# Kernel tuning notes

Measured on AMD Instinct MI355X. Metric: run time of the kernel, lower is better.

Reference implementation:

```python
import jax, jax.numpy as jnp
import numpy as np

B, I, O, G, D = 2048, 128, 128, 8, 2  # batch, input_dim, output_dim, num_grids, num_dim (complex algebra)
RHO = 1.0
EPS = 1e-5  # BatchNorm1d default eps
GRID_MIN, GRID_MAX = -2.0, 2.0


def _make_cayley():
    # Complex-number geometric algebra: metric=[-1], basis {1, e1}, e1*e1 = -1.
    # (a*b)_z = sum_{x,y} a_x b_y C[x,y,z]
    C = np.zeros((2, 2, 2), dtype=np.float32)
    C[0, 0, 0] = 1.0
    C[0, 1, 1] = 1.0
    C[1, 0, 1] = 1.0
    C[1, 1, 0] = -1.0
    return jnp.asarray(C)


def _make_grid():
    # create_grid2d_full: real varies along axis 0, imag along axis 1 -> (G, G, 2)
    g = jnp.linspace(GRID_MIN, GRID_MAX, G)
    gr, gi = jnp.meshgrid(g, g, indexing='ij')
    return jnp.stack((gr, gi), axis=-1)


def setup_inputs() -> dict:
    key = jax.random.key(0)
    k1, k2 = jax.random.split(key)
    x = jax.random.normal(k1, (B, I, D), dtype=jnp.float32)
    weights = jax.random.normal(k2, (I, O, G, G, D), dtype=jnp.float32)
    silu_weight = jnp.ones((I, O, D), dtype=jnp.float32)
    silu_bias = jnp.zeros((I, O, D), dtype=jnp.float32)
    gamma = jnp.ones((D,), dtype=jnp.float32)   # BatchNorm weight (componentwise)
    beta = jnp.zeros((D,), dtype=jnp.float32)   # BatchNorm bias
    return {
        'x': x,
        'weights': weights,
        'silu_weight': silu_weight,
        'silu_bias': silu_bias,
        'gamma': gamma,
        'beta': beta,
        'grid': _make_grid(),
        'cayley': _make_cayley(),
    }


def reference(x, weights, silu_weight, silu_bias, gamma, beta, grid, cayley):
    # RBF expansion: exp(-||x - grid_point||^2 / rho), complex-algebra norm^2 = a^2 + b^2
    diff = x[:, :, None, None, :] - grid[None, None, :, :, :]        # (B, I, G, G, D)
    rbf = jnp.exp(-jnp.sum(diff * diff, axis=-1) / RHO)              # (B, I, G, G)
    # grid-weight contraction
    res = jnp.einsum('biuv,iouvx->biox', rbf, weights)               # (B, I, O, D)
    # componentwise SiLU branch with Cayley-table (complex) multiplication
    s = jax.nn.silu(x)                                               # (B, I, D)
    sv = jnp.einsum('iox,biy,xyz->bioz', silu_weight, s, cayley)     # (B, I, O, D)
    sv = sv + silu_bias
    out = jnp.sum(res + sv, axis=1)                                  # (B, O, D) -- 'biox->box'
    # componentwise BatchNorm (training mode): stats over (B, O) per component
    mean = jnp.mean(out, axis=(0, 1))
    var = jnp.var(out, axis=(0, 1))
    out = gamma * (out - mean) * jax.lax.rsqrt(var + EPS) + beta
    return out
```

## Files before the change

### kernel.cpp

```cpp
#include <hip/hip_runtime.h>
#include <stdint.h>

typedef unsigned short u16;
typedef __attribute__((ext_vector_type(8))) short bf16x8;
typedef __attribute__((ext_vector_type(4))) float f32x4;

#define B_      2048
#define I_      128
#define O_      128
#define K_MAIN  8192
#define K_TOT   8448
#define N_      256
#define BO      262144

#define A_OFF      0u
#define A_BYTES    (2048u*8448u*2u)
#define W_OFF      (A_OFF + A_BYTES)
#define W_BYTES    (256u*8448u*2u)
#define OUTP_OFF   (W_OFF + W_BYTES)
#define OUTP_BYTES (524288u*4u)
#define BSUM_OFF   (OUTP_OFF + OUTP_BYTES)
#define STATS_OFF  (BSUM_OFF + 1024u)

__device__ __forceinline__ float bf2f(u16 u) {
    union { unsigned int i; float f; } c; c.i = ((unsigned int)u) << 16; return c.f;
}
__device__ __forceinline__ u16 f2bf(float f) {
    unsigned int u = __float_as_uint(f);
    return (u16)((u + 0x7fffu + ((u >> 16) & 1u)) >> 16);
}
__device__ __forceinline__ float loadF(const void* p, long idx, bool isbf) {
    return isbf ? bf2f(((const u16*)p)[idx]) : ((const float*)p)[idx];
}

#define GLD16(gsrc, ldst) __builtin_amdgcn_global_load_lds( \
    (const __attribute__((address_space(1))) void*)(gsrc),  \
    (__attribute__((address_space(3))) void*)(ldst), 16, 0, 0)

__global__ void zero_ws(float* out_pre, float* stats, float* bsum) {
    int gid = blockIdx.x * 256 + threadIdx.x;
    out_pre[gid] = 0.0f;
    if (gid < 256) bsum[gid] = 0.0f;
    if (gid < 4) stats[gid] = 0.0f;
}

__global__ __launch_bounds__(256) void pack_a(const void* x, const void* grd, u16* A,
                                              const u16* flag) {
    bool isbf = (flag[0] == 0x3F80u);
    __shared__ float sg[8];
    if (threadIdx.x < 8)
        sg[threadIdx.x] = loadF(grd, (long)threadIdx.x * 16, isbf);
    __syncthreads();
    int p = blockIdx.x * 256 + threadIdx.x;
    int b = p >> 7, i = p & 127;
    float xr = loadF(x, (long)p * 2, isbf);
    float xi = loadF(x, (long)p * 2 + 1, isbf);
    float er[8], ei[8];
#pragma unroll
    for (int j = 0; j < 8; ++j) {
        float dr = xr - sg[j]; er[j] = __expf(-dr * dr);
        float di = xi - sg[j]; ei[j] = __expf(-di * di);
    }
    unsigned int outp[32];
#pragma unroll
    for (int u = 0; u < 8; ++u)
#pragma unroll
        for (int v = 0; v < 8; v += 2) {
            unsigned int lo = f2bf(er[u] * ei[v]);
            unsigned int hi = f2bf(er[u] * ei[v + 1]);
            outp[(u * 8 + v) >> 1] = lo | (hi << 16);
        }
    u16* dst = A + (size_t)b * K_TOT + i * 64;
#pragma unroll
    for (int q = 0; q < 8; ++q)
        ((uint4*)dst)[q] = ((const uint4*)outp)[q];
    float s0 = xr / (1.0f + __expf(-xr));
    float s1 = xi / (1.0f + __expf(-xi));
    unsigned int packed = (unsigned int)f2bf(s0) | ((unsigned int)f2bf(s1) << 16);
    *(unsigned int*)(A + (size_t)b * K_TOT + K_MAIN + 2 * i) = packed;
}

__global__ __launch_bounds__(256) void pack_w(const void* wgt, const void* sw, u16* W,
                                              const u16* flag) {
    bool isbf = (flag[0] == 0x3F80u);
    if (blockIdx.x < 1024) {
        int gid = blockIdx.x * 256 + threadIdx.x;
        int t8 = gid & 15;
        int io = gid >> 4;
        int i = io >> 7, o = io & 127;
        int base = t8 * 8;
        int u = base >> 4, v0 = (base & 15) >> 1;
        long off = ((long)i * 128 + o) * 128 + base;
        float f[8];
        if (isbf) {
            uint4 raw = *(const uint4*)((const u16*)wgt + off);
            const u16* h = (const u16*)&raw;
#pragma unroll
            for (int j = 0; j < 8; ++j) f[j] = bf2f(h[j]);
        } else {
            float4 a = *(const float4*)((const float*)wgt + off);
            float4 bq = *(const float4*)((const float*)wgt + off + 4);
            f[0]=a.x; f[1]=a.y; f[2]=a.z; f[3]=a.w;
            f[4]=bq.x; f[5]=bq.y; f[6]=bq.z; f[7]=bq.w;
        }
        u16 re[4], im[4];
#pragma unroll
        for (int j = 0; j < 4; ++j) { re[j] = f2bf(f[2*j]); im[j] = f2bf(f[2*j+1]); }
        int k = i * 64 + u * 8 + v0;
        *(uint2*)&W[(size_t)(2*o)     * K_TOT + k] = *(const uint2*)re;
        *(uint2*)&W[(size_t)(2*o + 1) * K_TOT + k] = *(const uint2*)im;
    } else {
        int e = (blockIdx.x - 1024) * 256 + threadIdx.x;
        int n = e >> 8, j = e & 255;
        int o = n >> 1, xc = n & 1;
        int i = j >> 1, c = j & 1;
        float swr = loadF(sw, (long)(i * 128 + o) * 2, isbf);
        float swi = loadF(sw, (long)(i * 128 + o) * 2 + 1, isbf);
        float v = (xc == 0) ? (c == 0 ? swr : -swi) : (c == 0 ? swi : swr);
        W[(size_t)n * K_TOT + K_MAIN + j] = f2bf(v);
    }
}

__global__ void bias_sum(const void* sb, float* bsum, const u16* flag) {
    bool isbf = (flag[0] == 0x3F80u);
    int n = threadIdx.x;
    int i0 = blockIdx.x * 8;
    float s = 0.0f;
#pragma unroll
    for (int j = 0; j < 8; ++j) s += loadF(sb, (long)(i0 + j) * 256 + n, isbf);
    atomicAdd(&bsum[n], s);
}

#define BM 128
#define BN 64
#define BK 64
#define NSPLIT 8
#define KSTEPS 132

__global__ __launch_bounds__(256, 2) void gemm_k(const u16* __restrict__ A,
                                                 const u16* __restrict__ W,
                                                 float* out_pre) {
    __shared__ u16 As[BM * BK];
    __shared__ u16 Bs[BN * BK];
    int tid = threadIdx.x, lane = tid & 63, w = tid >> 6;
    int wm = w >> 1, wn = w & 1;
    int m0 = blockIdx.y * BM;
    int n0 = blockIdx.x * BN;
    int s = blockIdx.z;
    int kbeg = (KSTEPS * s) / NSPLIT, kend = (KSTEPS * (s + 1)) / NSPLIT;

    f32x4 zero = {0.f, 0.f, 0.f, 0.f};
    f32x4 acc[4][2];
#pragma unroll
    for (int mt = 0; mt < 4; ++mt)
#pragma unroll
        for (int nt = 0; nt < 2; ++nt) acc[mt][nt] = zero;

    int quad = lane >> 4, l16 = lane & 15;

    for (int kt = kbeg; kt < kend; ++kt) {
        int k0 = kt * BK;
#pragma unroll
        for (int j = 0; j < 4; ++j) {
            int c = (w * 4 + j) * 64 + lane;
            int row = c >> 3, col = c & 7;
            GLD16(A + (size_t)(m0 + row) * K_TOT + k0 + col * 8,
                  As + (size_t)(w * 4 + j) * 512);
        }
#pragma unroll
        for (int j = 0; j < 2; ++j) {
            int c = (w * 2 + j) * 64 + lane;
            int row = c >> 3, col = c & 7;
            GLD16(W + (size_t)(n0 + row) * K_TOT + k0 + col * 8,
                  Bs + (size_t)(w * 2 + j) * 512);
        }
        __syncthreads();
#pragma unroll
        for (int ks = 0; ks < 2; ++ks) {
            bf16x8 fa[4], fb[2];
#pragma unroll
            for (int mt = 0; mt < 4; ++mt)
                fa[mt] = *(const bf16x8*)&As[(wm * 64 + mt * 16 + l16) * BK + ks * 32 + quad * 8];
#pragma unroll
            for (int nt = 0; nt < 2; ++nt)
                fb[nt] = *(const bf16x8*)&Bs[(wn * 32 + nt * 16 + l16) * BK + ks * 32 + quad * 8];
#pragma unroll
            for (int mt = 0; mt < 4; ++mt)
#pragma unroll
                for (int nt = 0; nt < 2; ++nt)
                    acc[mt][nt] = __builtin_amdgcn_mfma_f32_16x16x32_bf16(
                        fa[mt], fb[nt], acc[mt][nt], 0, 0, 0);
        }
        __syncthreads();
    }
    int mbase = m0 + wm * 64 + quad * 4;
    int nbase = n0 + wn * 32 + l16;
#pragma unroll
    for (int mt = 0; mt < 4; ++mt)
#pragma unroll
        for (int nt = 0; nt < 2; ++nt) {
            int n = nbase + nt * 16;
#pragma unroll
            for (int r = 0; r < 4; ++r) {
                int m = mbase + mt * 16 + r;
                atomicAdd(&out_pre[(size_t)m * N_ + n], acc[mt][nt][r]);
            }
        }
}

__global__ void stats_k(const float* __restrict__ out_pre, const float* __restrict__ bsum,
                        float* stats) {
    int gid = blockIdx.x * 256 + threadIdx.x;
    int o = gid & 127;
    float vr = out_pre[(size_t)gid * 2]     + bsum[o * 2];
    float vi = out_pre[(size_t)gid * 2 + 1] + bsum[o * 2 + 1];
    float sr = vr, si = vi, qr = vr * vr, qi = vi * vi;
    for (int off = 32; off > 0; off >>= 1) {
        sr += __shfl_down(sr, off);
        si += __shfl_down(si, off);
        qr += __shfl_down(qr, off);
        qi += __shfl_down(qi, off);
    }
    __shared__ float red[4][4];
    int lane = threadIdx.x & 63, w = threadIdx.x >> 6;
    if (lane == 0) { red[w][0] = sr; red[w][1] = si; red[w][2] = qr; red[w][3] = qi; }
    __syncthreads();
    if (threadIdx.x < 4) {
        float t = red[0][threadIdx.x] + red[1][threadIdx.x] +
                  red[2][threadIdx.x] + red[3][threadIdx.x];
        atomicAdd(&stats[threadIdx.x], t);
    }
}

__global__ void norm_k(const float* __restrict__ out_pre, const float* __restrict__ bsum,
                       const float* __restrict__ stats, const void* gamma, const void* beta,
                       void* out, const u16* flag) {
    bool isbf = (flag[0] == 0x3F80u);
    int gid = blockIdx.x * 256 + threadIdx.x;
    int o = gid & 127;
    const float inv = 1.0f / (float)BO;
    float mr = stats[0] * inv, mi = stats[1] * inv;
    float varr = stats[2] * inv - mr * mr;
    float vari = stats[3] * inv - mi * mi;
    float gr = loadF(gamma, 0, isbf), gi = loadF(gamma, 1, isbf);
    float br = loadF(beta, 0, isbf),  bi = loadF(beta, 1, isbf);
    float scr = gr * rsqrtf(varr + 1e-5f);
    float sci = gi * rsqrtf(vari + 1e-5f);
    float vr = out_pre[(size_t)gid * 2]     + bsum[o * 2];
    float vi = out_pre[(size_t)gid * 2 + 1] + bsum[o * 2 + 1];
    float rr = (vr - mr) * scr + br;
    float ri = (vi - mi) * sci + bi;
    if (isbf) {
        unsigned int packed = (unsigned int)f2bf(rr) | ((unsigned int)f2bf(ri) << 16);
        *(unsigned int*)((u16*)out + (size_t)gid * 2) = packed;
    } else {
        ((float*)out)[(size_t)gid * 2]     = rr;
        ((float*)out)[(size_t)gid * 2 + 1] = ri;
    }
}

extern "C" void kernel_launch(void* const* d_in, const int* in_sizes, int n_in,
                              void* d_out, int out_size, void* d_ws, size_t ws_size,
                              hipStream_t stream) {
    const void* x     = d_in[0];
    const void* wgt   = d_in[1];
    const void* sw    = d_in[2];
    const void* sb    = d_in[3];
    const void* gamma = d_in[4];
    const void* beta  = d_in[5];
    const void* grd   = d_in[6];
    const u16* flag = (const u16*)gamma;

    uint8_t* ws = (uint8_t*)d_ws;
    u16*   A       = (u16*)(ws + A_OFF);
    u16*   W       = (u16*)(ws + W_OFF);
    float* out_pre = (float*)(ws + OUTP_OFF);
    float* bsum    = (float*)(ws + BSUM_OFF);
    float* stats   = (float*)(ws + STATS_OFF);

    zero_ws<<<2048, 256, 0, stream>>>(out_pre, stats, bsum);
    pack_a<<<1024, 256, 0, stream>>>(x, grd, A, flag);
    pack_w<<<1280, 256, 0, stream>>>(wgt, sw, W, flag);
    bias_sum<<<16, 256, 0, stream>>>(sb, bsum, flag);
    gemm_k<<<dim3(N_ / BN, B_ / BM, NSPLIT), 256, 0, stream>>>(A, W, out_pre);
    stats_k<<<1024, 256, 0, stream>>>(out_pre, bsum, stats);
    norm_k<<<1024, 256, 0, stream>>>(out_pre, bsum, stats, gamma, beta, d_out, flag);
}
```

Baseline: 144.2 us.

## Fuse RBF/SiLU feature generation into GEMM and replace atomics with split-K partial buffers

The RBF expansion and SiLU features are now generated directly into shared memory inside the GEMM, so the large packed A matrix (about 34 MB of bf16) is no longer written to and reread from global memory. The split-K atomicAdd accumulation is replaced by nine per-slice partial buffers that a stats kernel sums, which also removes the zeroing kernel. The bias-sum and stats initialisation are folded into pack_w, cutting the launch count. The trade-off is exp work recomputed redundantly per N-tile (four times), extra partial-buffer traffic, and a short ninth slice that adds imbalance.

```diff
diff --git a/kernel.cpp b/kernel.cpp
--- a/kernel.cpp
+++ b/kernel.cpp
@@ -12,14 +12,15 @@
 #define K_TOT   8448
 #define N_      256
 #define BO      262144
-
-#define A_OFF      0u
-#define A_BYTES    (2048u*8448u*2u)
-#define W_OFF      (A_OFF + A_BYTES)
+#define NSLICE  9
+
+#define W_OFF      0u
 #define W_BYTES    (256u*8448u*2u)
-#define OUTP_OFF   (W_OFF + W_BYTES)
-#define OUTP_BYTES (524288u*4u)
-#define BSUM_OFF   (OUTP_OFF + OUTP_BYTES)
+#define OUTPS_OFF  (W_OFF + W_BYTES)
+#define OUTPS_BYTES (9u*524288u*4u)
+#define OUTRED_OFF (OUTPS_OFF + OUTPS_BYTES)
+#define OUTRED_BYTES (524288u*4u)
+#define BSUM_OFF   (OUTRED_OFF + OUTRED_BYTES)
 #define STATS_OFF  (BSUM_OFF + 1024u)
 
 __device__ __forceinline__ float bf2f(u16 u) {
@@ -37,51 +38,9 @@
     (const __attribute__((address_space(1))) void*)(gsrc),  \
     (__attribute__((address_space(3))) void*)(ldst), 16, 0, 0)
 
-__global__ void zero_ws(float* out_pre, float* stats, float* bsum) {
-    int gid = blockIdx.x * 256 + threadIdx.x;
-    out_pre[gid] = 0.0f;
-    if (gid < 256) bsum[gid] = 0.0f;
-    if (gid < 4) stats[gid] = 0.0f;
-}
-
-__global__ __launch_bounds__(256) void pack_a(const void* x, const void* grd, u16* A,
-                                              const u16* flag) {
-    bool isbf = (flag[0] == 0x3F80u);
-    __shared__ float sg[8];
-    if (threadIdx.x < 8)
-        sg[threadIdx.x] = loadF(grd, (long)threadIdx.x * 16, isbf);
-    __syncthreads();
-    int p = blockIdx.x * 256 + threadIdx.x;
-    int b = p >> 7, i = p & 127;
-    float xr = loadF(x, (long)p * 2, isbf);
-    float xi = loadF(x, (long)p * 2 + 1, isbf);
-    float er[8], ei[8];
-#pragma unroll
-    for (int j = 0; j < 8; ++j) {
-        float dr = xr - sg[j]; er[j] = __expf(-dr * dr);
-        float di = xi - sg[j]; ei[j] = __expf(-di * di);
-    }
-    unsigned int outp[32];
-#pragma unroll
-    for (int u = 0; u < 8; ++u)
-#pragma unroll
-        for (int v = 0; v < 8; v += 2) {
-            unsigned int lo = f2bf(er[u] * ei[v]);
-            unsigned int hi = f2bf(er[u] * ei[v + 1]);
-            outp[(u * 8 + v) >> 1] = lo | (hi << 16);
-        }
-    u16* dst = A + (size_t)b * K_TOT + i * 64;
-#pragma unroll
-    for (int q = 0; q < 8; ++q)
-        ((uint4*)dst)[q] = ((const uint4*)outp)[q];
-    float s0 = xr / (1.0f + __expf(-xr));
-    float s1 = xi / (1.0f + __expf(-xi));
-    unsigned int packed = (unsigned int)f2bf(s0) | ((unsigned int)f2bf(s1) << 16);
-    *(unsigned int*)(A + (size_t)b * K_TOT + K_MAIN + 2 * i) = packed;
-}
-
-__global__ __launch_bounds__(256) void pack_w(const void* wgt, const void* sw, u16* W,
-                                              const u16* flag) {
+__global__ __launch_bounds__(256) void pack_w(const void* wgt, const void* sw,
+                                              const void* sb, u16* W, float* bsum,
+                                              float* stats, const u16* flag) {
     bool isbf = (flag[0] == 0x3F80u);
     if (blockIdx.x < 1024) {
         int gid = blockIdx.x * 256 + threadIdx.x;
@@ -109,7 +68,7 @@
         int k = i * 64 + u * 8 + v0;
         *(uint2*)&W[(size_t)(2*o)     * K_TOT + k] = *(const uint2*)re;
         *(uint2*)&W[(size_t)(2*o + 1) * K_TOT + k] = *(const uint2*)im;
-    } else {
+    } else if (blockIdx.x < 1280) {
         int e = (blockIdx.x - 1024) * 256 + threadIdx.x;
         int n = e >> 8, j = e & 255;
         int o = n >> 1, xc = n & 1;
@@ -118,36 +77,40 @@
         float swi = loadF(sw, (long)(i * 128 + o) * 2 + 1, isbf);
         float v = (xc == 0) ? (c == 0 ? swr : -swi) : (c == 0 ? swi : swr);
         W[(size_t)n * K_TOT + K_MAIN + j] = f2bf(v);
-    }
-}
-
-__global__ void bias_sum(const void* sb, float* bsum, const u16* flag) {
-    bool isbf = (flag[0] == 0x3F80u);
-    int n = threadIdx.x;
-    int i0 = blockIdx.x * 8;
-    float s = 0.0f;
-#pragma unroll
-    for (int j = 0; j < 8; ++j) s += loadF(sb, (long)(i0 + j) * 256 + n, isbf);
-    atomicAdd(&bsum[n], s);
+    } else {
+        int n = threadIdx.x;
+        float s = 0.0f;
+#pragma unroll 8
+        for (int i = 0; i < 128; ++i) s += loadF(sb, (long)i * 256 + n, isbf);
+        bsum[n] = s;
+        if (threadIdx.x < 4) stats[threadIdx.x] = 0.0f;
+    }
 }
 
 #define BM 128
 #define BN 64
 #define BK 64
-#define NSPLIT 8
-#define KSTEPS 132
-
-__global__ __launch_bounds__(256, 2) void gemm_k(const u16* __restrict__ A,
-                                                 const u16* __restrict__ W,
-                                                 float* out_pre) {
+
+__global__ __launch_bounds__(256, 2) void gemm_fused(const void* __restrict__ x,
+                                                     const void* __restrict__ grd,
+                                                     const u16* __restrict__ W,
+                                                     float* __restrict__ out_ps,
+                                                     const u16* flag) {
+    bool isbf = (flag[0] == 0x3F80u);
     __shared__ u16 As[BM * BK];
     __shared__ u16 Bs[BN * BK];
+    __shared__ float xs[128][17][2];
     int tid = threadIdx.x, lane = tid & 63, w = tid >> 6;
     int wm = w >> 1, wn = w & 1;
     int m0 = blockIdx.y * BM;
     int n0 = blockIdx.x * BN;
     int s = blockIdx.z;
-    int kbeg = (KSTEPS * s) / NSPLIT, kend = (KSTEPS * (s + 1)) / NSPLIT;
+    int quad = lane >> 4, l16 = lane & 15;
+    int mrow = tid >> 1, h = tid & 1;
+
+    float g[8];
+#pragma unroll
+    for (int j = 0; j < 8; ++j) g[j] = loadF(grd, (long)j * 16, isbf);
 
     f32x4 zero = {0.f, 0.f, 0.f, 0.f};
     f32x4 acc[4][2];
@@ -156,43 +119,105 @@
 #pragma unroll
         for (int nt = 0; nt < 2; ++nt) acc[mt][nt] = zero;
 
-    int quad = lane >> 4, l16 = lane & 15;
-
-    for (int kt = kbeg; kt < kend; ++kt) {
-        int k0 = kt * BK;
-#pragma unroll
-        for (int j = 0; j < 4; ++j) {
-            int c = (w * 4 + j) * 64 + lane;
-            int row = c >> 3, col = c & 7;
-            GLD16(A + (size_t)(m0 + row) * K_TOT + k0 + col * 8,
-                  As + (size_t)(w * 4 + j) * 512);
-        }
-#pragma unroll
-        for (int j = 0; j < 2; ++j) {
-            int c = (w * 2 + j) * 64 + lane;
-            int row = c >> 3, col = c & 7;
-            GLD16(W + (size_t)(n0 + row) * K_TOT + k0 + col * 8,
-                  Bs + (size_t)(w * 2 + j) * 512);
+    if (s < 8) {
+        {
+            long base = ((long)(m0 + mrow) * 128 + s * 16 + 8 * h) * 2;
+#pragma unroll
+            for (int e = 0; e < 16; ++e)
+                xs[mrow][8 * h + (e >> 1)][e & 1] = loadF(x, base + e, isbf);
         }
         __syncthreads();
-#pragma unroll
-        for (int ks = 0; ks < 2; ++ks) {
-            bf16x8 fa[4], fb[2];
-#pragma unroll
-            for (int mt = 0; mt < 4; ++mt)
-                fa[mt] = *(const bf16x8*)&As[(wm * 64 + mt * 16 + l16) * BK + ks * 32 + quad * 8];
-#pragma unroll
-            for (int nt = 0; nt < 2; ++nt)
-                fb[nt] = *(const bf16x8*)&Bs[(wn * 32 + nt * 16 + l16) * BK + ks * 32 + quad * 8];
-#pragma unroll
-            for (int mt = 0; mt < 4; ++mt)
+        for (int j = 0; j < 16; ++j) {
+            int k0 = (s * 16 + j) * 64;
+#pragma unroll
+            for (int jj = 0; jj < 2; ++jj) {
+                int c = (w * 2 + jj) * 64 + lane;
+                int row = c >> 3, col = c & 7;
+                GLD16(W + (size_t)(n0 + row) * K_TOT + k0 + col * 8,
+                      Bs + (size_t)(w * 2 + jj) * 512);
+            }
+            float xr = xs[mrow][j][0], xi = xs[mrow][j][1];
+            float ei[8];
+#pragma unroll
+            for (int v = 0; v < 8; ++v) { float d = xi - g[v]; ei[v] = __expf(-d * d); }
+            unsigned int op[16];
+#pragma unroll
+            for (int uu = 0; uu < 4; ++uu) {
+                float d = xr - g[4 * h + uu];
+                float er = __expf(-d * d);
+#pragma unroll
+                for (int v = 0; v < 8; v += 2) {
+                    unsigned int lo = f2bf(er * ei[v]);
+                    unsigned int hi = f2bf(er * ei[v + 1]);
+                    op[uu * 4 + (v >> 1)] = lo | (hi << 16);
+                }
+            }
+            u16* dst = As + mrow * 64 + 32 * h;
+#pragma unroll
+            for (int q = 0; q < 4; ++q) ((uint4*)dst)[q] = ((const uint4*)op)[q];
+            __syncthreads();
+#pragma unroll
+            for (int ks = 0; ks < 2; ++ks) {
+                bf16x8 fa[4], fb[2];
+#pragma unroll
+                for (int mt = 0; mt < 4; ++mt)
+                    fa[mt] = *(const bf16x8*)&As[(wm * 64 + mt * 16 + l16) * BK + ks * 32 + quad * 8];
 #pragma unroll
                 for (int nt = 0; nt < 2; ++nt)
-                    acc[mt][nt] = __builtin_amdgcn_mfma_f32_16x16x32_bf16(
-                        fa[mt], fb[nt], acc[mt][nt], 0, 0, 0);
-        }
-        __syncthreads();
-    }
+                    fb[nt] = *(const bf16x8*)&Bs[(wn * 32 + nt * 16 + l16) * BK + ks * 32 + quad * 8];
+#pragma unroll
+                for (int mt = 0; mt < 4; ++mt)
+#pragma unroll
+                    for (int nt = 0; nt < 2; ++nt)
+                        acc[mt][nt] = __builtin_amdgcn_mfma_f32_16x16x32_bf16(
+                            fa[mt], fb[nt], acc[mt][nt], 0, 0, 0);
+            }
+            __syncthreads();
+        }
+    } else {
+        for (int t = 0; t < 4; ++t) {
+            int k0 = K_MAIN + t * 64;
+#pragma unroll
+            for (int jj = 0; jj < 2; ++jj) {
+                int c = (w * 2 + jj) * 64 + lane;
+                int row = c >> 3, col = c & 7;
+                GLD16(W + (size_t)(n0 + row) * K_TOT + k0 + col * 8,
+                      Bs + (size_t)(w * 2 + jj) * 512);
+            }
+            long base = ((long)(m0 + mrow) * 128 + 32 * t) * 2 + 32 * h;
+            unsigned int op[16];
+#pragma unroll
+            for (int e = 0; e < 32; e += 2) {
+                float v0 = loadF(x, base + e, isbf);
+                float v1 = loadF(x, base + e + 1, isbf);
+                float s0 = v0 / (1.0f + __expf(-v0));
+                float s1 = v1 / (1.0f + __expf(-v1));
+                op[e >> 1] = (unsigned int)f2bf(s0) | ((unsigned int)f2bf(s1) << 16);
+            }
+            u16* dst = As + mrow * 64 + 32 * h;
+#pragma unroll
+            for (int q = 0; q < 4; ++q) ((uint4*)dst)[q] = ((const uint4*)op)[q];
+            __syncthreads();
+#pragma unroll
+            for (int ks = 0; ks < 2; ++ks) {
+                bf16x8 fa[4], fb[2];
+#pragma unroll
+                for (int mt = 0; mt < 4; ++mt)
+                    fa[mt] = *(const bf16x8*)&As[(wm * 64 + mt * 16 + l16) * BK + ks * 32 + quad * 8];
+#pragma unroll
+                for (int nt = 0; nt < 2; ++nt)
+                    fb[nt] = *(const bf16x8*)&Bs[(wn * 32 + nt * 16 + l16) * BK + ks * 32 + quad * 8];
+#pragma unroll
+                for (int mt = 0; mt < 4; ++mt)
+#pragma unroll
+                    for (int nt = 0; nt < 2; ++nt)
+                        acc[mt][nt] = __builtin_amdgcn_mfma_f32_16x16x32_bf16(
+                            fa[mt], fb[nt], acc[mt][nt], 0, 0, 0);
+            }
+            __syncthreads();
+        }
+    }
+    float* outp = out_ps + (size_t)s * 524288;
     int mbase = m0 + wm * 64 + quad * 4;
     int nbase = n0 + wn * 32 + l16;
 #pragma unroll
@@ -203,17 +228,24 @@
 #pragma unroll
             for (int r = 0; r < 4; ++r) {
                 int m = mbase + mt * 16 + r;
-                atomicAdd(&out_pre[(size_t)m * N_ + n], acc[mt][nt][r]);
-            }
-        }
-}
-
-__global__ void stats_k(const float* __restrict__ out_pre, const float* __restrict__ bsum,
-                        float* stats) {
+                outp[(size_t)m * N_ + n] = acc[mt][nt][r];
+            }
+        }
+}
+
+__global__ void stats_red(const float* __restrict__ out_ps, const float* __restrict__ bsum,
+                          float* __restrict__ out_red, float* stats) {
     int gid = blockIdx.x * 256 + threadIdx.x;
     int o = gid & 127;
-    float vr = out_pre[(size_t)gid * 2]     + bsum[o * 2];
-    float vi = out_pre[(size_t)gid * 2 + 1] + bsum[o * 2 + 1];
+    float vr = 0.f, vi = 0.f;
+#pragma unroll
+    for (int s = 0; s < NSLICE; ++s) {
+        float2 p = *(const float2*)(out_ps + (size_t)s * 524288 + (size_t)gid * 2);
+        vr += p.x; vi += p.y;
+    }
+    vr += bsum[o * 2]; vi += bsum[o * 2 + 1];
+    float2 ov; ov.x = vr; ov.y = vi;
+    *(float2*)(out_red + (size_t)gid * 2) = ov;
     float sr = vr, si = vi, qr = vr * vr, qi = vi * vi;
     for (int off = 32; off > 0; off >>= 1) {
         sr += __shfl_down(sr, off);
@@ -232,12 +264,10 @@
     }
 }
 
-__global__ void norm_k(const float* __restrict__ out_pre, const float* __restrict__ bsum,
-                       const float* __restrict__ stats, const void* gamma, const void* beta,
-                       void* out, const u16* flag) {
+__global__ void norm_k(const float* __restrict__ out_red, const float* __restrict__ stats,
+                       const void* gamma, const void* beta, void* out, const u16* flag) {
     bool isbf = (flag[0] == 0x3F80u);
     int gid = blockIdx.x * 256 + threadIdx.x;
-    int o = gid & 127;
     const float inv = 1.0f / (float)BO;
     float mr = stats[0] * inv, mi = stats[1] * inv;
     float varr = stats[2] * inv - mr * mr;
@@ -246,10 +276,9 @@
     float br = loadF(beta, 0, isbf),  bi = loadF(beta, 1, isbf);
     float scr = gr * rsqrtf(varr + 1e-5f);
     float sci = gi * rsqrtf(vari + 1e-5f);
-    float vr = out_pre[(size_t)gid * 2]     + bsum[o * 2];
-    float vi = out_pre[(size_t)gid * 2 + 1] + bsum[o * 2 + 1];
-    float rr = (vr - mr) * scr + br;
-    float ri = (vi - mi) * sci + bi;
+    float2 v = *(const float2*)(out_red + (size_t)gid * 2);
+    float rr = (v.x - mr) * scr + br;
+    float ri = (v.y - mi) * sci + bi;
     if (isbf) {
         unsigned int packed = (unsigned int)f2bf(rr) | ((unsigned int)f2bf(ri) << 16);
         *(unsigned int*)((u16*)out + (size_t)gid * 2) = packed;
@@ -272,17 +301,14 @@
     const u16* flag = (const u16*)gamma;
 
     uint8_t* ws = (uint8_t*)d_ws;
-    u16*   A       = (u16*)(ws + A_OFF);
     u16*   W       = (u16*)(ws + W_OFF);
-    float* out_pre = (float*)(ws + OUTP_OFF);
+    float* out_ps  = (float*)(ws + OUTPS_OFF);
+    float* out_red = (float*)(ws + OUTRED_OFF);
     float* bsum    = (float*)(ws + BSUM_OFF);
     float* stats   = (float*)(ws + STATS_OFF);
 
-    zero_ws<<<2048, 256, 0, stream>>>(out_pre, stats, bsum);
-    pack_a<<<1024, 256, 0, stream>>>(x, grd, A, flag);
-    pack_w<<<1280, 256, 0, stream>>>(wgt, sw, W, flag);
-    bias_sum<<<16, 256, 0, stream>>>(sb, bsum, flag);
-    gemm_k<<<dim3(N_ / BN, B_ / BM, NSPLIT), 256, 0, stream>>>(A, W, out_pre);
-    stats_k<<<1024, 256, 0, stream>>>(out_pre, bsum, stats);
-    norm_k<<<1024, 256, 0, stream>>>(out_pre, bsum, stats, gamma, beta, d_out, flag);
-}
+    pack_w<<<1281, 256, 0, stream>>>(wgt, sw, sb, W, bsum, stats, flag);
+    gemm_fused<<<dim3(N_ / BN, B_ / BM, NSLICE), 256, 0, stream>>>(x, grd, W, out_ps, flag);
+    stats_red<<<1024, 256, 0, stream>>>(out_ps, bsum, out_red, stats);
+    norm_k<<<1024, 256, 0, stream>>>(out_red, stats, gamma, beta, d_out, flag);
+}
```

After: 168.4 us. +16.8%, slower.
